# Performance work log

Measured on AMD Instinct MI355X. Metric: run time of the kernel, lower is better.

Reference implementation:

```python
import jax, jax.numpy as jnp
import numpy as np

RANK = 64
SCALING = 1.0 / RANK  # LoRAAdapter.scaling
TEMPERATURE = 1.0     # FusionConfig.gate_temperature


def setup_inputs() -> dict:
    key = jax.random.key(0)
    k_x, k_a, k_b, k_w = jax.random.split(key, 4)
    B_, S, D = 4, 2048, 2048
    E, R, O = 8, RANK, 2048
    x = jax.random.normal(k_x, (B_, S, D), dtype=jnp.float32)
    # lora_A weights [E, rank, d] (kaiming-uniform-ish scale); lora_B [E, out, rank]
    # NOTE: torch inits lora_B to zeros (degenerate output); we use small random
    # values so the reference exercises the full compute path.
    A = jax.random.normal(k_a, (E, R, D), dtype=jnp.float32) * (1.0 / np.sqrt(D))
    Bw = jax.random.normal(k_b, (E, O, R), dtype=jnp.float32) * 0.02
    Wr = jax.random.normal(k_w, (E, D), dtype=jnp.float32) * (1.0 / np.sqrt(D))
    br = jnp.zeros((E,), dtype=jnp.float32)
    return {"x": x, "A": A, "B": Bw, "Wr": Wr, "br": br}


def reference(x, A, B, Wr, br):
    batch, seq, d = x.shape
    E, out_dim = B.shape[0], B.shape[1]
    x_flat = x.reshape(-1, d)  # [N, d]

    # SparseRouter: top-1 routing
    logits = (x_flat @ Wr.T + br) / TEMPERATURE          # [N, E]
    probs = jax.nn.softmax(logits, axis=-1)              # [N, E]
    expert_idx = jnp.argmax(probs, axis=-1)              # [N] int
    expert_weight = jnp.max(probs, axis=-1)              # [N]

    # Per-expert LoRA: compute all experts densely, then select top-1 per token.
    # h: [N, E, r], y: [N, E, out]
    h = jnp.einsum('nd,erd->ner', x_flat, A)
    y = jnp.einsum('ner,eor->neo', h, B) * SCALING
    sel = jnp.take_along_axis(y, expert_idx[:, None, None], axis=1)[:, 0, :]  # [N, out]

    out_flat = sel * expert_weight[:, None]
    return out_flat.reshape(batch, seq, out_dim)
```

## Files before the change

kernel.cpp:

```cpp
#include <hip/hip_runtime.h>
#include <hip/hip_bf16.h>

#define NTOK 8192
#define DIM 2048
#define EXP 8
#define RK 64
#define OUTD 2048
#define SCALING (1.0f / 64.0f)
#define TTILE 32
#define MAXTILES (NTOK / TTILE)
#define JBINS 2
#define BK 128
#define MT (TTILE / 16)

typedef __attribute__((ext_vector_type(8))) short bf16x8;
typedef __attribute__((ext_vector_type(4))) short s16x4;
typedef __attribute__((ext_vector_type(4))) float f32x4;

__device__ __forceinline__ short f2bf(float f) {
    return __builtin_bit_cast(short, __float2bfloat16(f));
}

__device__ __forceinline__ bf16x8 load_cvt8(const float* __restrict__ p) {
    const float4 a = *(const float4*)(p);
    const float4 b = *(const float4*)(p + 4);
    bf16x8 r;
    r[0] = f2bf(a.x); r[1] = f2bf(a.y); r[2] = f2bf(a.z); r[3] = f2bf(a.w);
    r[4] = f2bf(b.x); r[5] = f2bf(b.y); r[6] = f2bf(b.z); r[7] = f2bf(b.w);
    return r;
}

__global__ void init_counts(int* __restrict__ counts) {
    if (threadIdx.x < EXP) counts[threadIdx.x] = 0;
}

__global__ __launch_bounds__(512) void router_kernel(
    const float* __restrict__ X, const float* __restrict__ Wr,
    const float* __restrict__ br, int* __restrict__ counts,
    float* __restrict__ wts, int* __restrict__ bucket) {
    __shared__ float4 Wlds[EXP * 512];
    __shared__ int ecnt[EXP];
    __shared__ int ebase[EXP];
    const int tid = threadIdx.x;
    const float4* W4 = (const float4*)Wr;
#pragma unroll
    for (int j = 0; j < 8; ++j) Wlds[tid + 512 * j] = W4[tid + 512 * j];
    if (tid < EXP) ecnt[tid] = 0;
    __syncthreads();

    const int wave = (blockIdx.x * 512 + tid) >> 6;
    const int lane = tid & 63;
    const int t0 = wave * 4;

    double acc[4][EXP];
#pragma unroll
    for (int t = 0; t < 4; ++t)
#pragma unroll
        for (int e = 0; e < EXP; ++e) acc[t][e] = 0.0;

    const float4* X4 = (const float4*)X;
    float4 xc0, xc1, xc2, xc3, xn0, xn1, xn2, xn3;
    xc0 = X4[(size_t)(t0 + 0) * 512 + lane];
    xc1 = X4[(size_t)(t0 + 1) * 512 + lane];
    xc2 = X4[(size_t)(t0 + 2) * 512 + lane];
    xc3 = X4[(size_t)(t0 + 3) * 512 + lane];

#pragma unroll
    for (int i = 0; i < 8; ++i) {
        if (i < 7) {
            const int cn = lane + 64 * (i + 1);
            xn0 = X4[(size_t)(t0 + 0) * 512 + cn];
            xn1 = X4[(size_t)(t0 + 1) * 512 + cn];
            xn2 = X4[(size_t)(t0 + 2) * 512 + cn];
            xn3 = X4[(size_t)(t0 + 3) * 512 + cn];
        }
        const int c = lane + 64 * i;
#pragma unroll
        for (int e = 0; e < EXP; ++e) {
            const float4 wv = Wlds[e * 512 + c];
            acc[0][e] += (double)xc0.x * wv.x + (double)xc0.y * wv.y +
                         (double)xc0.z * wv.z + (double)xc0.w * wv.w;
            acc[1][e] += (double)xc1.x * wv.x + (double)xc1.y * wv.y +
                         (double)xc1.z * wv.z + (double)xc1.w * wv.w;
            acc[2][e] += (double)xc2.x * wv.x + (double)xc2.y * wv.y +
                         (double)xc2.z * wv.z + (double)xc2.w * wv.w;
            acc[3][e] += (double)xc3.x * wv.x + (double)xc3.y * wv.y +
                         (double)xc3.z * wv.z + (double)xc3.w * wv.w;
        }
        xc0 = xn0; xc1 = xn1; xc2 = xn2; xc3 = xn3;
    }

#pragma unroll
    for (int t = 0; t < 4; ++t)
#pragma unroll
        for (int e = 0; e < EXP; ++e) {
            double v = acc[t][e];
#pragma unroll
            for (int off = 32; off >= 1; off >>= 1) v += __shfl_xor(v, off, 64);
            acc[t][e] = v;
        }

    __syncthreads();

    int n_l = -1, bi_l = 0, rank_l = 0;
#pragma unroll
    for (int t = 0; t < 4; ++t) {
        if (lane == t) {
            double lg[EXP];
#pragma unroll
            for (int e = 0; e < EXP; ++e) lg[e] = acc[t][e] + (double)br[e];
            double m = lg[0];
            int bi = 0;
#pragma unroll
            for (int e = 1; e < EXP; ++e)
                if (lg[e] > m) { m = lg[e]; bi = e; }
            float s = 0.f;
#pragma unroll
            for (int e = 0; e < EXP; ++e) s += __expf((float)(lg[e] - m));
            n_l = t0 + t;
            bi_l = bi;
            wts[n_l] = 1.0f / s;
            rank_l = atomicAdd(&ecnt[bi], 1);
        }
    }
    __syncthreads();
    if (tid < EXP) ebase[tid] = (ecnt[tid] > 0) ? atomicAdd(&counts[tid], ecnt[tid]) : 0;
    __syncthreads();
    if (n_l >= 0) bucket[bi_l * NTOK + ebase[bi_l] + rank_l] = n_l;
}

__global__ __launch_bounds__(256, 2) void moe_lora_kernel(
    const float* __restrict__ X, const float* __restrict__ A,
    const float* __restrict__ B, const int* __restrict__ counts,
    const float* __restrict__ wts, const int* __restrict__ bucket,
    float* __restrict__ out) {
    const int e = blockIdx.x >> 8;
    const int tile = blockIdx.x & 255;
    const int jbin = blockIdx.y;
    const int cnt = counts[e];
    const int base = tile * TTILE;
    if (base >= cnt) return;
    const int nt = min(TTILE, cnt - base);

    __shared__ int toks[TTILE];
    __shared__ float wt_s[TTILE];
    __shared__ short Xs[TTILE * BK];
    __shared__ short As[RK * BK];
    __shared__ short Hs[TTILE * RK];

    const int tid = threadIdx.x;
    if (tid < TTILE) {
        const int tk = bucket[e * NTOK + base + min(tid, nt - 1)];
        toks[tid] = tk;
        wt_s[tid] = wts[tk];
    }
    __syncthreads();

    const int wv = tid >> 6;
    const int lane = tid & 63;
    const int lrow = lane & 15;
    const int lk = lane >> 4;

    const float* Ae = A + (size_t)e * RK * DIM;
    const int scol = (tid & 31) * 4;
    const int srow = tid >> 5;

    f32x4 hacc[MT];
#pragma unroll
    for (int m = 0; m < MT; ++m) hacc[m] = (f32x4){0.f, 0.f, 0.f, 0.f};

    float4 xrA[4], arA[8], xrB[4], arB[8];

#define ISSUE(XR, AR, CH)                                                      \
    {                                                                          \
        const int k0_ = (CH)*BK;                                               \
        _Pragma("unroll") for (int i = 0; i < 4; ++i) {                        \
            const int row = i * 8 + srow;                                      \
            XR[i] = *(const float4*)(X + (size_t)toks[row] * DIM + k0_ + scol);\
        }                                                                      \
        _Pragma("unroll") for (int i = 0; i < 8; ++i) {                        \
            const int row = i * 8 + srow;                                      \
            AR[i] = *(const float4*)(Ae + (size_t)row * DIM + k0_ + scol);     \
        }                                                                      \
    }

#define STAGE(XR, AR)                                                          \
    {                                                                          \
        _Pragma("unroll") for (int i = 0; i < 4; ++i) {                        \
            const int row = i * 8 + srow;                                      \
            s16x4 hx = {f2bf(XR[i].x), f2bf(XR[i].y), f2bf(XR[i].z),           \
                        f2bf(XR[i].w)};                                        \
            *(s16x4*)((char*)Xs + ((row * 256 + scol * 2) ^ ((row & 7) << 4))) = hx; \
        }                                                                      \
        _Pragma("unroll") for (int i = 0; i < 8; ++i) {                        \
            const int row = i * 8 + srow;                                      \
            s16x4 ha = {f2bf(AR[i].x), f2bf(AR[i].y), f2bf(AR[i].z),           \
                        f2bf(AR[i].w)};                                        \
            *(s16x4*)((char*)As + ((row * 256 + scol * 2) ^ ((row & 7) << 4))) = ha; \
        }                                                                      \
    }

#define MFMA_CHUNK()                                                           \
    {                                                                          \
        _Pragma("unroll") for (int kk = 0; kk < 4; ++kk) {                     \
            const int cb = kk * 64 + lk * 16;                                  \
            const int ar_ = wv * 16 + lrow;                                    \
            const bf16x8 af = *(const bf16x8*)((char*)As +                     \
                ((ar_ * 256 + cb) ^ ((ar_ & 7) << 4)));                        \
            _Pragma("unroll") for (int m = 0; m < MT; ++m) {                   \
                const int xr_ = m * 16 + lrow;                                 \
                const bf16x8 xf = *(const bf16x8*)((char*)Xs +                 \
                    ((xr_ * 256 + cb) ^ ((xr_ & 7) << 4)));                    \
                hacc[m] = __builtin_amdgcn_mfma_f32_16x16x32_bf16(             \
                    xf, af, hacc[m], 0, 0, 0);                                 \
            }                                                                  \
        }                                                                      \
    }

    ISSUE(xrA, arA, 0);
#pragma unroll 1
    for (int ch = 0; ch < DIM / BK; ch += 2) {
        __syncthreads();
        STAGE(xrA, arA);
        ISSUE(xrB, arB, ch + 1);
        __syncthreads();
        MFMA_CHUNK();

        __syncthreads();
        STAGE(xrB, arB);
        if (ch + 2 < DIM / BK) ISSUE(xrA, arA, ch + 2);
        __syncthreads();
        MFMA_CHUNK();
    }
#undef ISSUE
#undef STAGE
#undef MFMA_CHUNK

#pragma unroll
    for (int m = 0; m < MT; ++m) {
#pragma unroll
        for (int reg = 0; reg < 4; ++reg) {
            const int t = m * 16 + lk * 4 + reg;
            const int r = wv * 16 + lrow;
            const int byte = ((t * RK + r) * 2) ^ ((t & 7) << 4);
            *(short*)((char*)Hs + byte) = f2bf(hacc[m][reg]);
        }
    }
    __syncthreads();

    bf16x8 hf[MT][2];
#pragma unroll
    for (int m = 0; m < MT; ++m)
#pragma unroll
        for (int k2 = 0; k2 < 2; ++k2) {
            const int t = m * 16 + lrow;
            const int r = k2 * 32 + lk * 8;
            const int byte = ((t * RK + r) * 2) ^ ((t & 7) << 4);
            hf[m][k2] = *(const bf16x8*)((char*)Hs + byte);
        }

    float scl[MT][4];
    int trow[MT][4];
    bool tok_ok[MT][4];
#pragma unroll
    for (int m = 0; m < MT; ++m)
#pragma unroll
        for (int reg = 0; reg < 4; ++reg) {
            const int t = m * 16 + lk * 4 + reg;
            scl[m][reg] = SCALING * wt_s[t];
            trow[m][reg] = toks[t];
            tok_ok[m][reg] = (t < nt);
        }

    const float* Be = B + (size_t)e * OUTD * RK;
    const int j0 = jbin * (OUTD / 64 / JBINS);
    for (int j = j0; j < j0 + OUTD / 64 / JBINS; ++j) {
        const int n = (wv + 4 * j) * 16;
        f32x4 yacc[MT];
#pragma unroll
        for (int m = 0; m < MT; ++m) yacc[m] = (f32x4){0.f, 0.f, 0.f, 0.f};
#pragma unroll
        for (int k2 = 0; k2 < 2; ++k2) {
            const bf16x8 bf =
                load_cvt8(Be + (size_t)(n + lrow) * RK + k2 * 32 + lk * 8);
#pragma unroll
            for (int m = 0; m < MT; ++m)
                yacc[m] = __builtin_amdgcn_mfma_f32_16x16x32_bf16(hf[m][k2], bf, yacc[m], 0, 0, 0);
        }
#pragma unroll
        for (int m = 0; m < MT; ++m) {
#pragma unroll
            for (int reg = 0; reg < 4; ++reg) {
                if (tok_ok[m][reg]) {
                    const float y = yacc[m][reg] * scl[m][reg];
                    out[(size_t)trow[m][reg] * OUTD + n + lrow] = y;
                }
            }
        }
    }
}

extern "C" void kernel_launch(void* const* d_in, const int* in_sizes, int n_in,
                              void* d_out, int out_size, void* d_ws, size_t ws_size,
                              hipStream_t stream) {
    const float* X = (const float*)d_in[0];
    const float* A = (const float*)d_in[1];
    const float* B = (const float*)d_in[2];
    const float* Wr = (const float*)d_in[3];
    const float* br = (const float*)d_in[4];
    float* out = (float*)d_out;

    int* counts = (int*)d_ws;
    float* wts = (float*)((char*)d_ws + 64);
    int* bucket = (int*)((char*)d_ws + 64 + NTOK * 4);

    init_counts<<<1, 64, 0, stream>>>(counts);
    router_kernel<<<NTOK / 32, 512, 0, stream>>>(X, Wr, br, counts, wts, bucket);
    dim3 grid(EXP * MAXTILES, JBINS);
    moe_lora_kernel<<<grid, 256, 0, stream>>>(X, A, B, counts, wts, bucket, out);
}
```

Before: 96.24 us.

## Double token tile to 64 with 512-thread blocks splitting rank and token halves

Raises the per-block token tile from 32 to 64 and the block size from 256 to 512 threads. The eight waves are split 4 ways over rank and 2 ways over token halves for the first GEMM, and each wave now handles 4 token m-tiles in the second GEMM. The aim is to amortize the A-matrix loads and B loads over twice as many tokens, halving the repeated A traffic per token. In exchange, blocks are larger with more register pressure, padding waste for partially filled experts grows, and the grid has fewer blocks.

```diff
diff --git a/kernel.cpp b/kernel.cpp
--- a/kernel.cpp
+++ b/kernel.cpp
@@ -7,11 +7,10 @@
 #define RK 64
 #define OUTD 2048
 #define SCALING (1.0f / 64.0f)
-#define TTILE 32
+#define TTILE 64
 #define MAXTILES (NTOK / TTILE)
 #define JBINS 2
 #define BK 128
-#define MT (TTILE / 16)
 
 typedef __attribute__((ext_vector_type(8))) short bf16x8;
 typedef __attribute__((ext_vector_type(4))) short s16x4;
@@ -129,13 +128,13 @@
     if (n_l >= 0) bucket[bi_l * NTOK + ebase[bi_l] + rank_l] = n_l;
 }
 
-__global__ __launch_bounds__(256, 2) void moe_lora_kernel(
+__global__ __launch_bounds__(512, 2) void moe_lora_kernel(
     const float* __restrict__ X, const float* __restrict__ A,
     const float* __restrict__ B, const int* __restrict__ counts,
     const float* __restrict__ wts, const int* __restrict__ bucket,
     float* __restrict__ out) {
-    const int e = blockIdx.x >> 8;
-    const int tile = blockIdx.x & 255;
+    const int e = blockIdx.x >> 7;
+    const int tile = blockIdx.x & 127;
     const int jbin = blockIdx.y;
     const int cnt = counts[e];
     const int base = tile * TTILE;
@@ -160,26 +159,25 @@
     const int lane = tid & 63;
     const int lrow = lane & 15;
     const int lk = lane >> 4;
+    const int rblk = wv & 3;
+    const int mh = wv >> 2;
 
     const float* Ae = A + (size_t)e * RK * DIM;
     const int scol = (tid & 31) * 4;
     const int srow = tid >> 5;
 
-    f32x4 hacc[MT];
-#pragma unroll
-    for (int m = 0; m < MT; ++m) hacc[m] = (f32x4){0.f, 0.f, 0.f, 0.f};
-
-    float4 xrA[4], arA[8], xrB[4], arB[8];
+    f32x4 hacc[2];
+#pragma unroll
+    for (int mm = 0; mm < 2; ++mm) hacc[mm] = (f32x4){0.f, 0.f, 0.f, 0.f};
+
+    float4 xrA[4], arA[4], xrB[4], arB[4];
 
 #define ISSUE(XR, AR, CH)                                                      \
     {                                                                          \
         const int k0_ = (CH)*BK;                                               \
         _Pragma("unroll") for (int i = 0; i < 4; ++i) {                        \
-            const int row = i * 8 + srow;                                      \
+            const int row = i * 16 + srow;                                     \
             XR[i] = *(const float4*)(X + (size_t)toks[row] * DIM + k0_ + scol);\
-        }                                                                      \
-        _Pragma("unroll") for (int i = 0; i < 8; ++i) {                        \
-            const int row = i * 8 + srow;                                      \
             AR[i] = *(const float4*)(Ae + (size_t)row * DIM + k0_ + scol);     \
         }                                                                      \
     }
@@ -187,13 +185,10 @@
 #define STAGE(XR, AR)                                                          \
     {                                                                          \
         _Pragma("unroll") for (int i = 0; i < 4; ++i) {                        \
-            const int row = i * 8 + srow;                                      \
+            const int row = i * 16 + srow;                                     \
             s16x4 hx = {f2bf(XR[i].x), f2bf(XR[i].y), f2bf(XR[i].z),           \
                         f2bf(XR[i].w)};                                        \
             *(s16x4*)((char*)Xs + ((row * 256 + scol * 2) ^ ((row & 7) << 4))) = hx; \
-        }                                                                      \
-        _Pragma("unroll") for (int i = 0; i < 8; ++i) {                        \
-            const int row = i * 8 + srow;                                      \
             s16x4 ha = {f2bf(AR[i].x), f2bf(AR[i].y), f2bf(AR[i].z),           \
                         f2bf(AR[i].w)};                                        \
             *(s16x4*)((char*)As + ((row * 256 + scol * 2) ^ ((row & 7) << 4))) = ha; \
@@ -204,15 +199,15 @@
     {                                                                          \
         _Pragma("unroll") for (int kk = 0; kk < 4; ++kk) {                     \
             const int cb = kk * 64 + lk * 16;                                  \
-            const int ar_ = wv * 16 + lrow;                                    \
+            const int ar_ = rblk * 16 + lrow;                                  \
             const bf16x8 af = *(const bf16x8*)((char*)As +                     \
                 ((ar_ * 256 + cb) ^ ((ar_ & 7) << 4)));                        \
-            _Pragma("unroll") for (int m = 0; m < MT; ++m) {                   \
-                const int xr_ = m * 16 + lrow;                                 \
+            _Pragma("unroll") for (int mm = 0; mm < 2; ++mm) {                 \
+                const int xr_ = (mh * 2 + mm) * 16 + lrow;                     \
                 const bf16x8 xf = *(const bf16x8*)((char*)Xs +                 \
                     ((xr_ * 256 + cb) ^ ((xr_ & 7) << 4)));                    \
-                hacc[m] = __builtin_amdgcn_mfma_f32_16x16x32_bf16(             \
-                    xf, af, hacc[m], 0, 0, 0);                                 \
+                hacc[mm] = __builtin_amdgcn_mfma_f32_16x16x32_bf16(            \
+                    xf, af, hacc[mm], 0, 0, 0);                                \
             }                                                                  \
         }                                                                      \
     }
@@ -237,20 +232,20 @@
 #undef MFMA_CHUNK
 
 #pragma unroll
-    for (int m = 0; m < MT; ++m) {
+    for (int mm = 0; mm < 2; ++mm) {
 #pragma unroll
         for (int reg = 0; reg < 4; ++reg) {
-            const int t = m * 16 + lk * 4 + reg;
-            const int r = wv * 16 + lrow;
+            const int t = (mh * 2 + mm) * 16 + lk * 4 + reg;
+            const int r = rblk * 16 + lrow;
             const int byte = ((t * RK + r) * 2) ^ ((t & 7) << 4);
-            *(short*)((char*)Hs + byte) = f2bf(hacc[m][reg]);
-        }
-    }
-    __syncthreads();
-
-    bf16x8 hf[MT][2];
-#pragma unroll
-    for (int m = 0; m < MT; ++m)
+            *(short*)((char*)Hs + byte) = f2bf(hacc[mm][reg]);
+        }
+    }
+    __syncthreads();
+
+    bf16x8 hf[4][2];
+#pragma unroll
+    for (int m = 0; m < 4; ++m)
 #pragma unroll
         for (int k2 = 0; k2 < 2; ++k2) {
             const int t = m * 16 + lrow;
@@ -259,11 +254,11 @@
             hf[m][k2] = *(const bf16x8*)((char*)Hs + byte);
         }
 
-    float scl[MT][4];
-    int trow[MT][4];
-    bool tok_ok[MT][4];
-#pragma unroll
-    for (int m = 0; m < MT; ++m)
+    float scl[4][4];
+    int trow[4][4];
+    bool tok_ok[4][4];
+#pragma unroll
+    for (int m = 0; m < 4; ++m)
 #pragma unroll
         for (int reg = 0; reg < 4; ++reg) {
             const int t = m * 16 + lk * 4 + reg;
@@ -273,22 +268,22 @@
         }
 
     const float* Be = B + (size_t)e * OUTD * RK;
-    const int j0 = jbin * (OUTD / 64 / JBINS);
-    for (int j = j0; j < j0 + OUTD / 64 / JBINS; ++j) {
-        const int n = (wv + 4 * j) * 16;
-        f32x4 yacc[MT];
-#pragma unroll
-        for (int m = 0; m < MT; ++m) yacc[m] = (f32x4){0.f, 0.f, 0.f, 0.f};
+    const int j0 = jbin * 8;
+    for (int j = j0; j < j0 + 8; ++j) {
+        const int n = (wv + 8 * j) * 16;
+        f32x4 yacc[4];
+#pragma unroll
+        for (int m = 0; m < 4; ++m) yacc[m] = (f32x4){0.f, 0.f, 0.f, 0.f};
 #pragma unroll
         for (int k2 = 0; k2 < 2; ++k2) {
             const bf16x8 bf =
                 load_cvt8(Be + (size_t)(n + lrow) * RK + k2 * 32 + lk * 8);
 #pragma unroll
-            for (int m = 0; m < MT; ++m)
+            for (int m = 0; m < 4; ++m)
                 yacc[m] = __builtin_amdgcn_mfma_f32_16x16x32_bf16(hf[m][k2], bf, yacc[m], 0, 0, 0);
         }
 #pragma unroll
-        for (int m = 0; m < MT; ++m) {
+        for (int m = 0; m < 4; ++m) {
 #pragma unroll
             for (int reg = 0; reg < 4; ++reg) {
                 if (tok_ok[m][reg]) {
@@ -317,5 +312,5 @@
     init_counts<<<1, 64, 0, stream>>>(counts);
     router_kernel<<<NTOK / 32, 512, 0, stream>>>(X, Wr, br, counts, wts, bucket);
     dim3 grid(EXP * MAXTILES, JBINS);
-    moe_lora_kernel<<<grid, 256, 0, stream>>>(X, A, B, counts, wts, bucket, out);
-}
+    moe_lora_kernel<<<grid, 512, 0, stream>>>(X, A, B, counts, wts, bucket, out);
+}
```

After: 104.0 us. 8.0% more time.
